# Kernel optimization log

Hardware: AMD Instinct MI355X
Metric: run time of the kernel (lower is better)

## Reference

```python
import jax, jax.numpy as jnp
import numpy as np

N_EMBD = 1024
N_HEAD = 16
HEAD_DIM = N_EMBD // N_HEAD
B, T = 4, 1024
EPS = 1e-5


def _linear_params(key, fan_in, fan_out):
    kw, kb = jax.random.split(key)
    bound = 1.0 / np.sqrt(fan_in)
    W = jax.random.uniform(kw, (fan_in, fan_out), minval=-bound, maxval=bound, dtype=jnp.float32)
    b = jax.random.uniform(kb, (fan_out,), minval=-bound, maxval=bound, dtype=jnp.float32)
    return W, b


def setup_inputs() -> dict:
    key = jax.random.key(0)
    ks = jax.random.split(key, 8)
    x = jax.random.normal(ks[0], (B, T, N_EMBD), dtype=jnp.float32)
    Wq, bq = _linear_params(ks[1], N_EMBD, N_EMBD)
    Wk, bk = _linear_params(ks[2], N_EMBD, N_EMBD)
    Wv, bv = _linear_params(ks[3], N_EMBD, N_EMBD)
    Wp, bp = _linear_params(ks[4], N_EMBD, N_EMBD)
    W1, b1 = _linear_params(ks[5], N_EMBD, 4 * N_EMBD)
    W2, b2 = _linear_params(ks[6], 4 * N_EMBD, N_EMBD)
    g1 = jnp.ones((N_EMBD,), jnp.float32); be1 = jnp.zeros((N_EMBD,), jnp.float32)
    g2 = jnp.ones((N_EMBD,), jnp.float32); be2 = jnp.zeros((N_EMBD,), jnp.float32)
    return {"x": x, "Wq": Wq, "bq": bq, "Wk": Wk, "bk": bk, "Wv": Wv, "bv": bv,
            "Wp": Wp, "bp": bp, "W1": W1, "b1": b1, "W2": W2, "b2": b2,
            "g1": g1, "be1": be1, "g2": g2, "be2": be2}


def _layernorm(x, g, b):
    mu = jnp.mean(x, axis=-1, keepdims=True)
    var = jnp.mean(jnp.square(x - mu), axis=-1, keepdims=True)
    return (x - mu) * jax.lax.rsqrt(var + EPS) * g + b


def _attention(x, Wq, bq, Wk, bk, Wv, bv, Wp, bp):
    Bsz, Tt, C = x.shape
    def heads(W, b):
        return (x @ W + b).reshape(Bsz, Tt, N_HEAD, HEAD_DIM).transpose(0, 2, 1, 3)  # [B,H,T,d]
    q, k, v = heads(Wq, bq), heads(Wk, bk), heads(Wv, bv)
    scores = jnp.einsum('bhqd,bhkd->bhqk', q, k) / np.sqrt(HEAD_DIM).astype(np.float32)
    causal = jnp.tril(jnp.ones((Tt, Tt), dtype=bool))
    scores = jnp.where(causal, scores, -jnp.inf)
    attn = jax.nn.softmax(scores, axis=-1)
    out = jnp.einsum('bhqk,bhkd->bhqd', attn, v)  # [B,H,T,d]
    out = out.transpose(0, 2, 1, 3).reshape(Bsz, Tt, C)
    return out @ Wp + bp


def _ff(x, W1, b1, W2, b2):
    h = jax.nn.gelu(x @ W1 + b1, approximate=False)  # torch nn.GELU default = exact erf
    return h @ W2 + b2


def reference(x, Wq, bq, Wk, bk, Wv, bv, Wp, bp, W1, b1, W2, b2, g1, be1, g2, be2):
    x = x + _attention(_layernorm(x, g1, be1), Wq, bq, Wk, bk, Wv, bv, Wp, bp)
    x = x + _ff(_layernorm(x, g2, be2), W1, b1, W2, b2)
    return x
```

## Files before the change

kernel.cpp:

```cpp
#include <hip/hip_runtime.h>
#include <hip/hip_bf16.h>

typedef __attribute__((ext_vector_type(8))) __bf16 bf16x8;
typedef __attribute__((ext_vector_type(4))) float f32x4;
typedef __attribute__((ext_vector_type(4))) unsigned short u16x4;
typedef unsigned short u16;

#define AS3(p) ((__attribute__((address_space(3))) void*)(p))
#define AS1(p) ((const __attribute__((address_space(1))) void*)(p))

__device__ __forceinline__ u16 f2b(float f) {
    __hip_bfloat16 h = __float2bfloat16(f);
    return __builtin_bit_cast(u16, h);
}

__device__ __forceinline__ float gelu_exact(float v) {
    const float z = v * 0.70710678118654752f;
    const float a = fabsf(z);
    const float t = __builtin_amdgcn_rcpf(1.0f + 0.3275911f * a);
    float p = 1.061405429f;
    p = p * t - 1.453152027f;
    p = p * t + 1.421413741f;
    p = p * t - 0.284496736f;
    p = p * t + 0.254829592f;
    p = p * t;
    float erfv = 1.0f - p * __expf(-a * a);
    erfv = copysignf(erfv, z);
    return 0.5f * v * (1.0f + erfv);
}

__global__ __launch_bounds__(256) void transpose_w(
    const float* __restrict__ W, u16* __restrict__ WT, int K, int N)
{
    __shared__ u16 tile[32][33];
    const int tx = threadIdx.x & 31, ty = threadIdx.x >> 5;
    const int n0 = blockIdx.x * 32, k0 = blockIdx.y * 32;
    #pragma unroll
    for (int p = 0; p < 4; ++p)
        tile[ty + p * 8][tx] = f2b(W[(size_t)(k0 + ty + p * 8) * N + n0 + tx]);
    __syncthreads();
    #pragma unroll
    for (int p = 0; p < 4; ++p)
        WT[(size_t)(n0 + ty + p * 8) * K + k0 + tx] = tile[tx][ty + p * 8];
}

__global__ __launch_bounds__(256) void transpose_w3(
    const float* __restrict__ W0, const float* __restrict__ W1,
    const float* __restrict__ W2, u16* __restrict__ WT)
{
    __shared__ u16 tile[32][33];
    const int z = blockIdx.z;
    const float* W = (z == 0) ? W0 : (z == 1) ? W1 : W2;
    u16* dst = WT + (size_t)z * 1024 * 1024;
    const int tx = threadIdx.x & 31, ty = threadIdx.x >> 5;
    const int n0 = blockIdx.x * 32, k0 = blockIdx.y * 32;
    #pragma unroll
    for (int p = 0; p < 4; ++p)
        tile[ty + p * 8][tx] = f2b(W[(size_t)(k0 + ty + p * 8) * 1024 + n0 + tx]);
    __syncthreads();
    #pragma unroll
    for (int p = 0; p < 4; ++p)
        dst[(size_t)(n0 + ty + p * 8) * 1024 + k0 + tx] = tile[tx][ty + p * 8];
}

__global__ __launch_bounds__(256) void ln_bf16(
    const float* __restrict__ xin, const float* __restrict__ gam,
    const float* __restrict__ bet, u16* __restrict__ yout)
{
    __shared__ float red[8];
    const int row = blockIdx.x, tid = threadIdx.x;
    float4 v = ((const float4*)(xin + (size_t)row * 1024))[tid];
    float s = v.x + v.y + v.z + v.w;
    #pragma unroll
    for (int o = 32; o > 0; o >>= 1) s += __shfl_xor(s, o, 64);
    if ((tid & 63) == 0) red[tid >> 6] = s;
    __syncthreads();
    const float mu = (red[0] + red[1] + red[2] + red[3]) * (1.f / 1024.f);
    const float dx = v.x - mu, dy = v.y - mu, dz = v.z - mu, dw = v.w - mu;
    float sq = dx * dx + dy * dy + dz * dz + dw * dw;
    #pragma unroll
    for (int o = 32; o > 0; o >>= 1) sq += __shfl_xor(sq, o, 64);
    if ((tid & 63) == 0) red[4 + (tid >> 6)] = sq;
    __syncthreads();
    const float var = (red[4] + red[5] + red[6] + red[7]) * (1.f / 1024.f);
    const float inv = rsqrtf(var + 1e-5f);
    const float4 G = ((const float4*)gam)[tid];
    const float4 Bt = ((const float4*)bet)[tid];
    u16x4 o;
    o[0] = f2b(dx * inv * G.x + Bt.x);
    o[1] = f2b(dy * inv * G.y + Bt.y);
    o[2] = f2b(dz * inv * G.z + Bt.z);
    o[3] = f2b(dw * inv * G.w + Bt.w);
    ((u16x4*)(yout + (size_t)row * 1024))[tid] = o;
}

template <int MODE, int BN>
__global__ __launch_bounds__(256) void gemm_bf16(
    const u16* __restrict__ A, const u16* __restrict__ BT,
    const float* __restrict__ b0, const float* __restrict__ b1,
    const float* __restrict__ b2, const float* __restrict__ resid,
    void* __restrict__ outp, int M, int N, int K)
{
    constexpr int NI = BN / 32;
    constexpr int AELEM = 128 * 64;
    constexpr int BELEM = BN * 64;
    __shared__ u16 Asm[3 * AELEM];
    __shared__ u16 Bsm[3 * BELEM];
    const int tid = threadIdx.x;
    const int lane = tid & 63, wid = tid >> 6;
    const int bm0 = blockIdx.x * 128, bn0 = blockIdx.y * BN;
    const int wm = wid >> 1, wn = wid & 1;
    const int g = lane >> 4, l16 = lane & 15;
    const int srow = lane >> 3;
    const int sslot = (lane & 7) ^ srow;

    f32x4 acc[4][NI] = {};

    const u16* aBase = A + (size_t)bm0 * K + sslot * 8;
    const u16* bBase = BT + (size_t)bn0 * K + sslot * 8;

    auto stage = [&](int kt, int buf) {
        u16* adst = Asm + buf * AELEM;
        u16* bdst = Bsm + buf * BELEM;
        #pragma unroll
        for (int j = 0; j < 4; ++j) {
            const int inst = wid * 4 + j;
            const int row = inst * 8 + srow;
            __builtin_amdgcn_global_load_lds(AS1(aBase + (size_t)row * K + kt),
                                             AS3(adst + inst * 512), 16, 0, 0);
        }
        #pragma unroll
        for (int j = 0; j < NI; ++j) {
            const int inst = wid * NI + j;
            const int row = inst * 8 + srow;
            __builtin_amdgcn_global_load_lds(AS1(bBase + (size_t)row * K + kt),
                                             AS3(bdst + inst * 512), 16, 0, 0);
        }
    };

    const int nt = K / 64;
    stage(0, 0);
    stage(64, 1);
    int cur = 0, pre = 2;

    for (int t = 0; t < nt; ++t) {
        if (t + 1 < nt) {
            if constexpr (NI == 2) asm volatile("s_waitcnt vmcnt(6)" ::: "memory");
            else                   asm volatile("s_waitcnt vmcnt(8)" ::: "memory");
        } else {
            asm volatile("s_waitcnt vmcnt(0)" ::: "memory");
        }
        __builtin_amdgcn_s_barrier();
        __builtin_amdgcn_sched_barrier(0);

        const u16* asrc = Asm + cur * AELEM;
        const u16* bsrc = Bsm + cur * BELEM;
        bf16x8 af[2][4], bfr[2][NI];
        #pragma unroll
        for (int ks = 0; ks < 2; ++ks) {
            #pragma unroll
            for (int mi = 0; mi < 4; ++mi) {
                const int r = wm * 64 + mi * 16 + l16;
                const int slot = (g + 4 * ks) ^ (r & 7);
                af[ks][mi] = *(const bf16x8*)(asrc + r * 64 + slot * 8);
            }
            #pragma unroll
            for (int ni = 0; ni < NI; ++ni) {
                const int r = wn * (BN / 2) + ni * 16 + l16;
                const int slot = (g + 4 * ks) ^ (r & 7);
                bfr[ks][ni] = *(const bf16x8*)(bsrc + r * 64 + slot * 8);
            }
        }
        if (t + 2 < nt) stage((t + 2) * 64, pre);

        #pragma unroll
        for (int ks = 0; ks < 2; ++ks)
            #pragma unroll
            for (int mi = 0; mi < 4; ++mi)
                #pragma unroll
                for (int ni = 0; ni < NI; ++ni)
                    acc[mi][ni] = __builtin_amdgcn_mfma_f32_16x16x32_bf16(
                        af[ks][mi], bfr[ks][ni], acc[mi][ni], 0, 0, 0);

        pre = cur;
        cur = (cur == 2) ? 0 : cur + 1;
    }

    #pragma unroll
    for (int mi = 0; mi < 4; ++mi) {
        #pragma unroll
        for (int ni = 0; ni < NI; ++ni) {
            #pragma unroll
            for (int j = 0; j < 4; ++j) {
                const int m = bm0 + wm * 64 + mi * 16 + g * 4 + j;
                const int n = bn0 + wn * (BN / 2) + ni * 16 + l16;
                float v = acc[mi][ni][j];
                if constexpr (MODE == 0) {
                    const float bias = (n < 1024) ? b0[n]
                                      : (n < 2048) ? b1[n - 1024] : b2[n - 2048];
                    ((u16*)outp)[(size_t)m * N + n] = f2b(v + bias);
                } else if constexpr (MODE == 1) {
                    ((float*)outp)[(size_t)m * N + n] =
                        v + b0[n] + resid[(size_t)m * N + n];
                } else {
                    ((u16*)outp)[(size_t)m * N + n] = f2b(gelu_exact(v + b0[n]));
                }
            }
        }
    }
}

__global__ __launch_bounds__(256) void attn_fwd(
    const u16* __restrict__ qkv, u16* __restrict__ outp)
{
    __shared__ u16 Ksm[64 * 72];
    __shared__ u16 Vsm[64 * 72];
    __shared__ u16 Psm[4][16 * 72];
    const int tid = threadIdx.x, lane = tid & 63, w = tid >> 6;
    const int lin = blockIdx.y * 8 + blockIdx.x;
    const int xq = (lin >> 3) & 7;
    const int bh = (((lin >> 6) & 7) << 3) | (lin & 7);
    const int b = bh >> 4, h = bh & 15;
    const int g = lane >> 4, l16 = lane & 15;
    const int skv = tid >> 4;
    const int sd4 = (tid & 15) * 4;

    const u16* kvb = qkv + (size_t)(b * 1024) * 3072 + 1024 + h * 64;

    u16x4 kreg[4], vreg[4];
    auto issue = [&](int kv0) {
        const u16* kb = kvb + (size_t)kv0 * 3072;
        #pragma unroll
        for (int i = 0; i < 4; ++i)
            kreg[i] = *(const u16x4*)(kb + (size_t)(skv + 16 * i) * 3072 + sd4);
        #pragma unroll
        for (int i = 0; i < 4; ++i)
            vreg[i] = *(const u16x4*)(kb + (size_t)(4 * skv + i) * 3072 + 1024 + sd4);
    };

    #pragma unroll
    for (int half = 0; half < 2; ++half) {
        const int qt = half ? (15 - xq) : xq;
        const int q0 = qt * 64;

        bf16x8 qf0, qf1;
        {
            const u16* qp = qkv + (size_t)(b * 1024 + q0 + w * 16 + l16) * 3072
                            + h * 64 + g * 8;
            qf0 = *(const bf16x8*)qp;
            qf1 = *(const bf16x8*)(qp + 32);
        }
        float m_run[4] = {-1e30f, -1e30f, -1e30f, -1e30f};
        float l_run[4] = {0.f, 0.f, 0.f, 0.f};
        f32x4 oacc[4] = {};

        issue(0);

        for (int kvt = 0; kvt <= qt; ++kvt) {
            const int kv0 = kvt * 64;
            __syncthreads();
            #pragma unroll
            for (int i = 0; i < 4; ++i)
                *(u16x4*)(Ksm + (skv + 16 * i) * 72 + sd4) = kreg[i];
            #pragma unroll
            for (int j = 0; j < 4; ++j) {
                u16x4 t;
                t[0] = vreg[0][j]; t[1] = vreg[1][j];
                t[2] = vreg[2][j]; t[3] = vreg[3][j];
                *(u16x4*)(Vsm + (sd4 + j) * 72 + 4 * skv) = t;
            }
            __syncthreads();
            if (kvt < qt) issue(kv0 + 64);

            f32x4 s[4];
            #pragma unroll
            for (int t = 0; t < 4; ++t) {
                const bf16x8 kf0 = *(const bf16x8*)(Ksm + (t * 16 + l16) * 72 + g * 8);
                const bf16x8 kf1 = *(const bf16x8*)(Ksm + (t * 16 + l16) * 72 + 32 + g * 8);
                f32x4 z = {};
                z = __builtin_amdgcn_mfma_f32_16x16x32_bf16(qf0, kf0, z, 0, 0, 0);
                z = __builtin_amdgcn_mfma_f32_16x16x32_bf16(qf1, kf1, z, 0, 0, 0);
                s[t] = z;
            }
            float mx[4] = {-1e30f, -1e30f, -1e30f, -1e30f};
            #pragma unroll
            for (int t = 0; t < 4; ++t)
                #pragma unroll
                for (int j = 0; j < 4; ++j) {
                    const int qrow = q0 + w * 16 + g * 4 + j;
                    const int kvc = kv0 + t * 16 + l16;
                    float v = s[t][j] * 0.125f;
                    if (kvc > qrow) v = -1e30f;
                    s[t][j] = v;
                    mx[j] = fmaxf(mx[j], v);
                }
            #pragma unroll
            for (int o = 1; o < 16; o <<= 1)
                #pragma unroll
                for (int j = 0; j < 4; ++j)
                    mx[j] = fmaxf(mx[j], __shfl_xor(mx[j], o, 16));
            float alpha[4], rs[4];
            #pragma unroll
            for (int j = 0; j < 4; ++j) {
                const float mn = fmaxf(m_run[j], mx[j]);
                alpha[j] = __expf(m_run[j] - mn);
                m_run[j] = mn;
                rs[j] = 0.f;
            }
            #pragma unroll
            for (int t = 0; t < 4; ++t)
                #pragma unroll
                for (int j = 0; j < 4; ++j) {
                    const float p = __expf(s[t][j] - m_run[j]);
                    s[t][j] = p;
                    rs[j] += p;
                }
            #pragma unroll
            for (int o = 1; o < 16; o <<= 1)
                #pragma unroll
                for (int j = 0; j < 4; ++j)
                    rs[j] += __shfl_xor(rs[j], o, 16);
            #pragma unroll
            for (int j = 0; j < 4; ++j)
                l_run[j] = l_run[j] * alpha[j] + rs[j];
            #pragma unroll
            for (int dt = 0; dt < 4; ++dt)
                #pragma unroll
                for (int j = 0; j < 4; ++j)
                    oacc[dt][j] *= alpha[j];
            #pragma unroll
            for (int t = 0; t < 4; ++t)
                #pragma unroll
                for (int j = 0; j < 4; ++j)
                    Psm[w][(g * 4 + j) * 72 + t * 16 + l16] = f2b(s[t][j]);
            const bf16x8 pf0 = *(const bf16x8*)(&Psm[w][l16 * 72 + g * 8]);
            const bf16x8 pf1 = *(const bf16x8*)(&Psm[w][l16 * 72 + 32 + g * 8]);
            #pragma unroll
            for (int dt = 0; dt < 4; ++dt) {
                const bf16x8 vf0 = *(const bf16x8*)(Vsm + (dt * 16 + l16) * 72 + g * 8);
                const bf16x8 vf1 = *(const bf16x8*)(Vsm + (dt * 16 + l16) * 72 + 32 + g * 8);
                oacc[dt] = __builtin_amdgcn_mfma_f32_16x16x32_bf16(pf0, vf0, oacc[dt], 0, 0, 0);
                oacc[dt] = __builtin_amdgcn_mfma_f32_16x16x32_bf16(pf1, vf1, oacc[dt], 0, 0, 0);
            }
        }
        #pragma unroll
        for (int dt = 0; dt < 4; ++dt)
            #pragma unroll
            for (int j = 0; j < 4; ++j) {
                const int m = b * 1024 + q0 + w * 16 + g * 4 + j;
                const int col = h * 64 + dt * 16 + l16;
                outp[(size_t)m * 1024 + col] = f2b(oacc[dt][j] / l_run[j]);
            }
    }
}

extern "C" void kernel_launch(void* const* d_in, const int* in_sizes, int n_in,
                              void* d_out, int out_size, void* d_ws, size_t ws_size,
                              hipStream_t stream)
{
    const float* x   = (const float*)d_in[0];
    const float* Wq  = (const float*)d_in[1];
    const float* bq  = (const float*)d_in[2];
    const float* Wk  = (const float*)d_in[3];
    const float* bk  = (const float*)d_in[4];
    const float* Wv  = (const float*)d_in[5];
    const float* bv  = (const float*)d_in[6];
    const float* Wp  = (const float*)d_in[7];
    const float* bp  = (const float*)d_in[8];
    const float* W1  = (const float*)d_in[9];
    const float* b1  = (const float*)d_in[10];
    const float* W2  = (const float*)d_in[11];
    const float* b2  = (const float*)d_in[12];
    const float* g1  = (const float*)d_in[13];
    const float* be1 = (const float*)d_in[14];
    const float* g2  = (const float*)d_in[15];
    const float* be2 = (const float*)d_in[16];

    char* ws = (char*)d_ws;
    const size_t MB = 1024 * 1024;
    u16*   ln_buf = (u16*)(ws);
    u16*   qkv    = (u16*)(ws + 8 * MB);
    u16*   attn_o = (u16*)(ws + 32 * MB);
    float* x1     = (float*)(ws + 40 * MB);
    u16*   hbuf   = (u16*)(ws + 56 * MB);
    u16*   wqkvT  = (u16*)(ws + 88 * MB);
    u16*   wpT    = (u16*)(ws + 94 * MB);
    u16*   w1T    = (u16*)(ws + 96 * MB);
    u16*   w2T    = (u16*)(ws + 104 * MB);

    transpose_w3<<<dim3(32, 32, 3), 256, 0, stream>>>(Wq, Wk, Wv, wqkvT);
    transpose_w<<<dim3(32, 32), 256, 0, stream>>>(Wp, wpT, 1024, 1024);
    transpose_w<<<dim3(128, 32), 256, 0, stream>>>(W1, w1T, 1024, 4096);
    transpose_w<<<dim3(32, 128), 256, 0, stream>>>(W2, w2T, 4096, 1024);

    ln_bf16<<<4096, 256, 0, stream>>>(x, g1, be1, ln_buf);
    gemm_bf16<0, 64><<<dim3(32, 48), 256, 0, stream>>>(
        ln_buf, wqkvT, bq, bk, bv, nullptr, qkv, 4096, 3072, 1024);
    attn_fwd<<<dim3(8, 64), 256, 0, stream>>>(qkv, attn_o);
    gemm_bf16<1, 64><<<dim3(32, 16), 256, 0, stream>>>(
        attn_o, wpT, bp, nullptr, nullptr, x, x1, 4096, 1024, 1024);
    ln_bf16<<<4096, 256, 0, stream>>>(x1, g2, be2, ln_buf);
    gemm_bf16<2, 64><<<dim3(32, 64), 256, 0, stream>>>(
        ln_buf, w1T, b1, nullptr, nullptr, nullptr, hbuf, 4096, 4096, 1024);
    gemm_bf16<1, 64><<<dim3(32, 16), 256, 0, stream>>>(
        hbuf, w2T, b2, nullptr, nullptr, x1, (float*)d_out, 4096, 1024, 4096);
}
```

Baseline: 210.0 us.

## Retile GEMMs to larger N tiles with K=32 stages and XCD-aware block mapping

Reworks the bf16 GEMM tiling. Tiles go from 128xBN (BN=64) with K-step 64 to BMx128 (BM=256 or 128) with K-step 32, and a new LDS swizzle matches the 32-wide rows. Blocks are remapped through a 1D grid so that consecutive tiles land on the same XCD, and launch bounds now set a minimum occupancy. The goal is more operand reuse per loaded byte and better L2 locality. In exchange each stage has less MFMA work to hide load latency, and register pressure rises under the occupancy bound.

```diff
diff --git a/kernel.cpp b/kernel.cpp
--- a/kernel.cpp
+++ b/kernel.cpp
@@ -94,59 +94,65 @@
     ((u16x4*)(yout + (size_t)row * 1024))[tid] = o;
 }
 
-template <int MODE, int BN>
-__global__ __launch_bounds__(256) void gemm_bf16(
+template <int MODE, int BM>
+__global__ __launch_bounds__(256, (BM == 128 ? 3 : 2)) void gemm_bf16(
     const u16* __restrict__ A, const u16* __restrict__ BT,
     const float* __restrict__ b0, const float* __restrict__ b1,
     const float* __restrict__ b2, const float* __restrict__ resid,
     void* __restrict__ outp, int M, int N, int K)
 {
-    constexpr int NI = BN / 32;
-    constexpr int AELEM = 128 * 64;
-    constexpr int BELEM = BN * 64;
+    constexpr int WM = BM / 2;
+    constexpr int MI = WM / 16;
+    constexpr int NI = 4;
+    constexpr int AJ = BM / 64;
+    constexpr int AELEM = BM * 32;
+    constexpr int BELEM = 128 * 32;
     __shared__ u16 Asm[3 * AELEM];
     __shared__ u16 Bsm[3 * BELEM];
+
     const int tid = threadIdx.x;
     const int lane = tid & 63, wid = tid >> 6;
-    const int bm0 = blockIdx.x * 128, bn0 = blockIdx.y * BN;
     const int wm = wid >> 1, wn = wid & 1;
     const int g = lane >> 4, l16 = lane & 15;
-    const int srow = lane >> 3;
-    const int sslot = (lane & 7) ^ srow;
-
-    f32x4 acc[4][NI] = {};
-
-    const u16* aBase = A + (size_t)bm0 * K + sslot * 8;
-    const u16* bBase = BT + (size_t)bn0 * K + sslot * 8;
+    const int sx = (l16 >> 1) & 3;
+    const int sslot = (lane & 3) ^ ((lane >> 3) & 3);
+
+    const int nBN = N >> 7;
+    const int cpx = gridDim.x >> 3;
+    const int wg = (blockIdx.x & 7) * cpx + (blockIdx.x >> 3);
+    const int bm0 = (wg / nBN) * BM, bn0 = (wg % nBN) * 128;
+
+    f32x4 acc[MI][NI] = {};
+
+    const u16* aBase = A + (size_t)(bm0 + (lane >> 2)) * K + sslot * 8;
+    const u16* bBase = BT + (size_t)(bn0 + (lane >> 2)) * K + sslot * 8;
 
     auto stage = [&](int kt, int buf) {
-        u16* adst = Asm + buf * AELEM;
-        u16* bdst = Bsm + buf * BELEM;
-        #pragma unroll
-        for (int j = 0; j < 4; ++j) {
-            const int inst = wid * 4 + j;
-            const int row = inst * 8 + srow;
-            __builtin_amdgcn_global_load_lds(AS1(aBase + (size_t)row * K + kt),
-                                             AS3(adst + inst * 512), 16, 0, 0);
-        }
-        #pragma unroll
-        for (int j = 0; j < NI; ++j) {
-            const int inst = wid * NI + j;
-            const int row = inst * 8 + srow;
-            __builtin_amdgcn_global_load_lds(AS1(bBase + (size_t)row * K + kt),
-                                             AS3(bdst + inst * 512), 16, 0, 0);
+        u16* adst = Asm + buf * AELEM + lane * 8;
+        u16* bdst = Bsm + buf * BELEM + lane * 8;
+        #pragma unroll
+        for (int j = 0; j < AJ; ++j) {
+            const int ia = wid * AJ + j;
+            __builtin_amdgcn_global_load_lds(AS1(aBase + (size_t)(ia * 16) * K + kt),
+                                             AS3(adst + ia * 512), 16, 0, 0);
+        }
+        #pragma unroll
+        for (int j = 0; j < 2; ++j) {
+            const int ib = wid * 2 + j;
+            __builtin_amdgcn_global_load_lds(AS1(bBase + (size_t)(ib * 16) * K + kt),
+                                             AS3(bdst + ib * 512), 16, 0, 0);
         }
     };
 
-    const int nt = K / 64;
+    const int nt = K / 32;
     stage(0, 0);
-    stage(64, 1);
+    stage(32, 1);
     int cur = 0, pre = 2;
 
     for (int t = 0; t < nt; ++t) {
         if (t + 1 < nt) {
-            if constexpr (NI == 2) asm volatile("s_waitcnt vmcnt(6)" ::: "memory");
-            else                   asm volatile("s_waitcnt vmcnt(8)" ::: "memory");
+            if constexpr (BM == 256) asm volatile("s_waitcnt vmcnt(6)" ::: "memory");
+            else                     asm volatile("s_waitcnt vmcnt(4)" ::: "memory");
         } else {
             asm volatile("s_waitcnt vmcnt(0)" ::: "memory");
         }
@@ -155,45 +161,38 @@
 
         const u16* asrc = Asm + cur * AELEM;
         const u16* bsrc = Bsm + cur * BELEM;
-        bf16x8 af[2][4], bfr[2][NI];
-        #pragma unroll
-        for (int ks = 0; ks < 2; ++ks) {
-            #pragma unroll
-            for (int mi = 0; mi < 4; ++mi) {
-                const int r = wm * 64 + mi * 16 + l16;
-                const int slot = (g + 4 * ks) ^ (r & 7);
-                af[ks][mi] = *(const bf16x8*)(asrc + r * 64 + slot * 8);
-            }
-            #pragma unroll
-            for (int ni = 0; ni < NI; ++ni) {
-                const int r = wn * (BN / 2) + ni * 16 + l16;
-                const int slot = (g + 4 * ks) ^ (r & 7);
-                bfr[ks][ni] = *(const bf16x8*)(bsrc + r * 64 + slot * 8);
-            }
-        }
-        if (t + 2 < nt) stage((t + 2) * 64, pre);
-
-        #pragma unroll
-        for (int ks = 0; ks < 2; ++ks)
-            #pragma unroll
-            for (int mi = 0; mi < 4; ++mi)
-                #pragma unroll
-                for (int ni = 0; ni < NI; ++ni)
-                    acc[mi][ni] = __builtin_amdgcn_mfma_f32_16x16x32_bf16(
-                        af[ks][mi], bfr[ks][ni], acc[mi][ni], 0, 0, 0);
+        bf16x8 af[MI], bfr[NI];
+        #pragma unroll
+        for (int mi = 0; mi < MI; ++mi) {
+            const int r = wm * WM + mi * 16 + l16;
+            af[mi] = *(const bf16x8*)(asrc + r * 32 + ((g ^ sx) << 3));
+        }
+        #pragma unroll
+        for (int ni = 0; ni < NI; ++ni) {
+            const int c = wn * 64 + ni * 16 + l16;
+            bfr[ni] = *(const bf16x8*)(bsrc + c * 32 + ((g ^ sx) << 3));
+        }
+        if (t + 2 < nt) stage((t + 2) * 32, pre);
+
+        #pragma unroll
+        for (int mi = 0; mi < MI; ++mi)
+            #pragma unroll
+            for (int ni = 0; ni < NI; ++ni)
+                acc[mi][ni] = __builtin_amdgcn_mfma_f32_16x16x32_bf16(
+                    af[mi], bfr[ni], acc[mi][ni], 0, 0, 0);
 
         pre = cur;
         cur = (cur == 2) ? 0 : cur + 1;
     }
 
     #pragma unroll
-    for (int mi = 0; mi < 4; ++mi) {
+    for (int mi = 0; mi < MI; ++mi) {
         #pragma unroll
         for (int ni = 0; ni < NI; ++ni) {
             #pragma unroll
             for (int j = 0; j < 4; ++j) {
-                const int m = bm0 + wm * 64 + mi * 16 + g * 4 + j;
-                const int n = bn0 + wn * (BN / 2) + ni * 16 + l16;
+                const int m = bm0 + wm * WM + mi * 16 + g * 4 + j;
+                const int n = bn0 + wn * 64 + ni * 16 + l16;
                 float v = acc[mi][ni][j];
                 if constexpr (MODE == 0) {
                     const float bias = (n < 1024) ? b0[n]
@@ -394,14 +393,14 @@
     transpose_w<<<dim3(32, 128), 256, 0, stream>>>(W2, w2T, 4096, 1024);
 
     ln_bf16<<<4096, 256, 0, stream>>>(x, g1, be1, ln_buf);
-    gemm_bf16<0, 64><<<dim3(32, 48), 256, 0, stream>>>(
+    gemm_bf16<0, 256><<<384, 256, 0, stream>>>(
         ln_buf, wqkvT, bq, bk, bv, nullptr, qkv, 4096, 3072, 1024);
     attn_fwd<<<dim3(8, 64), 256, 0, stream>>>(qkv, attn_o);
-    gemm_bf16<1, 64><<<dim3(32, 16), 256, 0, stream>>>(
+    gemm_bf16<1, 128><<<256, 256, 0, stream>>>(
         attn_o, wpT, bp, nullptr, nullptr, x, x1, 4096, 1024, 1024);
     ln_bf16<<<4096, 256, 0, stream>>>(x1, g2, be2, ln_buf);
-    gemm_bf16<2, 64><<<dim3(32, 64), 256, 0, stream>>>(
+    gemm_bf16<2, 256><<<512, 256, 0, stream>>>(
         ln_buf, w1T, b1, nullptr, nullptr, nullptr, hbuf, 4096, 4096, 1024);
-    gemm_bf16<1, 64><<<dim3(32, 16), 256, 0, stream>>>(
+    gemm_bf16<1, 128><<<256, 256, 0, stream>>>(
         hbuf, w2T, b2, nullptr, nullptr, x1, (float*)d_out, 4096, 1024, 4096);
 }
```

Result: slower. 228.2 us (+8.7%).
